# Kernel optimization log

Hardware: AMD Instinct MI355X
Metric: run time of the kernel (lower is better)

The kernel has to match this reference:

```python
import jax, jax.numpy as jnp
import numpy as np

MC = 16384
IND_T = 96
N_MAT = 4
N_STRIKES = 21


def _init_linear(key, fan_in, fan_out, prefix=()):
    k1, k2 = jax.random.split(key)
    lim = 1.0 / np.sqrt(fan_in)
    W = jax.random.uniform(k1, prefix + (fan_in, fan_out), minval=-lim, maxval=lim, dtype=jnp.float32)
    b = jax.random.uniform(k2, prefix + (fan_out,), minval=-lim, maxval=lim, dtype=jnp.float32)
    return W, b


def setup_inputs() -> dict:
    key = jax.random.key(0)
    ks = jax.random.split(key, 14)
    z = jax.random.normal(ks[0], (MC, IND_T), dtype=jnp.float32)
    zz = jax.random.normal(ks[1], (MC, IND_T), dtype=jnp.float32)
    timegrid = jnp.arange(IND_T + 1, dtype=jnp.float32) / 365.0  # daily grid
    maturities = jnp.array([24, 48, 72, 96], dtype=jnp.int32)    # in days
    strikes = jnp.linspace(0.8, 1.2, N_STRIKES, dtype=jnp.float32)
    sv_W1, sv_b1 = _init_linear(ks[2], 3, 100)
    sv_W2, sv_b2 = _init_linear(ks[3], 100, 100)
    sv_W3, sv_b3 = _init_linear(ks[4], 100, 1)
    vh_W1, vh_b1 = _init_linear(ks[5], 2, 20, (N_MAT,))
    vh_W2, vh_b2 = _init_linear(ks[6], 20, N_STRIKES, (N_MAT,))
    vd_W1, vd_b1 = _init_linear(ks[7], 1, 20)
    vd_W2, vd_b2 = _init_linear(ks[8], 20, 1)
    vv_W1, vv_b1 = _init_linear(ks[9], 1, 20)
    vv_W2, vv_b2 = _init_linear(ks[10], 20, 1)
    v0 = jax.random.uniform(ks[11], (1,), dtype=jnp.float32) * 0.1
    rho = jnp.ones((1,), dtype=jnp.float32) * -2.0
    return dict(S0=jnp.float32(1.0), rate=jnp.float32(0.05), z=z, zz=zz,
                timegrid=timegrid, strikes=strikes, v0=v0, rho=rho,
                sv_W1=sv_W1, sv_b1=sv_b1, sv_W2=sv_W2, sv_b2=sv_b2, sv_W3=sv_W3, sv_b3=sv_b3,
                vh_W1=vh_W1, vh_b1=vh_b1, vh_W2=vh_W2, vh_b2=vh_b2,
                vd_W1=vd_W1, vd_b1=vd_b1, vd_W2=vd_W2, vd_b2=vd_b2,
                vv_W1=vv_W1, vv_b1=vv_b1, vv_W2=vv_W2, vv_b2=vv_b2,
                maturities=maturities)


def reference(S0, rate, z, zz, timegrid, strikes, v0, rho,
              sv_W1, sv_b1, sv_W2, sv_b2, sv_W3, sv_b3,
              vh_W1, vh_b1, vh_W2, vh_b2,
              vd_W1, vd_b1, vd_W2, vd_b2,
              vv_W1, vv_b1, vv_W2, vv_b2,
              maturities):
    sg = jax.lax.stop_gradient
    mc = z.shape[0]
    n_mat = vh_W1.shape[0]
    n_strikes = strikes.shape[0]

    def s_vol(x):  # [MC,3] -> [MC,1], softplus output
        h1 = jax.nn.relu(x @ sv_W1 + sv_b1)
        h2 = jax.nn.relu(h1 @ sv_W2 + sv_b2)
        return jax.nn.softplus(h2 @ sv_W3 + sv_b3)

    def v_drift(v):  # [MC,1] -> [MC,1]
        return jax.nn.relu(v @ vd_W1 + vd_b1) @ vd_W2 + vd_b2

    def v_vol(v):  # [MC,1] -> [MC,1], softplus output
        return jax.nn.softplus(jax.nn.relu(v @ vv_W1 + vv_b1) @ vv_W2 + vv_b2)

    def vanilla_hedge_all(x):  # [MC,2] -> [MC, n_strikes, n_mat] (one net per maturity)
        h1 = jax.nn.relu(jnp.einsum('mi,kio->kmo', x, vh_W1) + vh_b1[:, None, :])
        out = jax.nn.softplus(jnp.einsum('kmo,koj->kmj', h1, vh_W2) + vh_b2[:, None, :])
        return jnp.transpose(out, (1, 2, 0))

    rho_t = jnp.tanh(rho)[0]
    days = jnp.round(timegrid * 365.0).astype(jnp.int32)       # [IND_T+1]
    le = days[1:, None] <= maturities[None, :]                  # [IND_T, n_mat]
    idx_net = jnp.argmax(le, axis=1)                            # first live maturity per step
    is_mat = jnp.any(days[1:, None] == maturities[None, :], axis=1)
    mat_idx = jnp.arange(n_mat)

    Slog0 = jnp.log(jnp.full((mc, 1), S0, dtype=jnp.float32))
    V0 = jnp.full((mc, 1), 1.0, dtype=jnp.float32) * jax.nn.sigmoid(v0)[0] * 0.5
    cv0 = jnp.zeros((mc, n_strikes, n_mat), dtype=jnp.float32)
    pv0 = jnp.zeros((n_mat, n_strikes), dtype=jnp.float32)

    xs = (z.T[:, :, None], zz.T[:, :, None], timegrid[:-1], timegrid[1:], idx_net, is_mat)

    def step(carry, x):
        Slog_old, V_old, cv, pv_h, pv_var = carry
        z_i, zz_i, t0, t1, idx, im = x
        h = t1 - t0
        sqh = jnp.sqrt(h)
        dW = sqh * z_i                                          # [MC,1]
        dB = rho_t * dW + jnp.sqrt(1.0 - rho_t ** 2) * sqh * zz_i
        ones_t = jnp.full((mc, 1), 1.0, dtype=jnp.float32) * t0
        pd = s_vol(jnp.concatenate([ones_t, Slog_old, V_old], axis=1))  # price diffusion
        cv_fwd = vanilla_hedge_all(jnp.concatenate([ones_t, sg(Slog_old)], axis=1))
        V_new = V_old + v_drift(V_old) * h + v_vol(V_old) * dB
        drift = rate - 0.5 * pd ** 2
        diff = pd * dW
        drift_c = 1.0 + jnp.abs(sg(drift)) * sqh                # tamed Euler
        diff_c = 1.0 + jnp.abs(sg(pd)) * sqh
        Slog_new = Slog_old + drift * h / drift_c + diff / diff_c
        S_new = jnp.exp(Slog_new)
        S_old = jnp.exp(Slog_old)
        dS = jnp.exp(-rate * t1) * S_new - jnp.exp(-rate * t0) * S_old  # [MC,1]
        mask = (mat_idx >= idx).astype(cv.dtype)                # live maturities only
        cv = cv + mask[None, None, :] * cv_fwd * sg(dS)[:, :, None]
        # hedged vanilla (call) prices collected at maturity steps
        payoff = jnp.exp(-rate * t1) * jnp.maximum(S_new - strikes[None, :], 0.0)
        price = payoff - cv[:, :, idx]                          # [MC, n_strikes]
        pv = jnp.mean(price, axis=0)
        pvar = jnp.var(price, axis=0, ddof=1)
        sel = (mat_idx == idx)[:, None] & im
        pv_h = jnp.where(sel, pv[None, :], pv_h)
        pv_var = jnp.where(sel, pvar[None, :], pv_var)
        return (Slog_new, V_new, cv, pv_h, pv_var), None

    (_, _, _, pv_h, pv_var), _ = jax.lax.scan(step, (Slog0, V0, cv0, pv0, pv0), xs)
    return jnp.stack([pv_h, pv_var])  # [2, n_mat, n_strikes]
```

## Files before the change

### kernel.cpp

```cpp
#include <hip/hip_runtime.h>
#include <hip/hip_bf16.h>
#include <math.h>


#define MC      16384
#define NSTEP   96
#define BLOCK   1024
#define NGROUP  256
#define NPAIR   84

typedef short bf16x8 __attribute__((ext_vector_type(8)));
typedef float f32x4  __attribute__((ext_vector_type(4)));

union U8 { uint4 u; bf16x8 v; };
union BF2U { __hip_bfloat162 b; unsigned u; };

__device__ __forceinline__ unsigned bf16rne(float x) {
    unsigned u = __float_as_uint(x);
    return (u + 0x7FFFu + ((u >> 16) & 1u)) >> 16;
}
__device__ __forceinline__ unsigned pk2(float lo, float hi) {
    BF2U t; t.b = __float22bfloat162_rn(make_float2(lo, hi));
    return t.u;
}
__device__ __forceinline__ float sp(float x) {
    return fmaxf(x, 0.f) + __logf(1.f + __expf(-fabsf(x)));
}

__global__ __launch_bounds__(BLOCK, 4)
void lsv_sim(const float* __restrict__ S0p,   const float* __restrict__ ratep,
             const float* __restrict__ z,     const float* __restrict__ zzg,
             const float* __restrict__ strikesg,
             const float* __restrict__ v0p,   const float* __restrict__ rhop,
             const float* __restrict__ svW1,  const float* __restrict__ svb1,
             const float* __restrict__ svW2,  const float* __restrict__ svb2,
             const float* __restrict__ svW3,  const float* __restrict__ svb3,
             const float* __restrict__ vhW1,  const float* __restrict__ vhb1,
             const float* __restrict__ vhW2,  const float* __restrict__ vhb2,
             const float* __restrict__ vdW1,  const float* __restrict__ vdb1,
             const float* __restrict__ vdW2,  const float* __restrict__ vdb2,
             const float* __restrict__ vvW1,  const float* __restrict__ vvb1,
             const float* __restrict__ vvW2,  const float* __restrict__ vvb2,
             const int*   __restrict__ mats,
             float* __restrict__ psum, float* __restrict__ psq)
{
    __shared__ __align__(16) unsigned short H1c[16 * 64 * 8];
    __shared__ __align__(16) float W1f[16 * 32];
    __shared__ __align__(16) float WH1f[16 * 32];
    __shared__ __align__(16) float B2T[128], W3T[128];
    __shared__ float RED[64 * 4];
    __shared__ float VDl[2][64], VVl[2][64];
    __shared__ float PSs[4][32], PSq[4][32];
    __shared__ float VW[128];

    const int tid  = threadIdx.x;
    const int lane = tid & 63;
    const int w    = __builtin_amdgcn_readfirstlane(tid >> 6);
    const int quad = lane >> 4;
    const int col  = lane & 15;
    const int gpath = blockIdx.x * 64 + lane;

    const int pt = w & 3;
    const int jg = w >> 2;
    const int hm = w >> 2;

    for (int e = tid; e < 128; e += BLOCK) {
        float v = 0.f;
        if      (e < 20)             v = vdW1[e];
        else if (e < 40)             v = vdb1[e - 20];
        else if (e < 60)             v = vdW2[e - 40];
        else if (e >= 64 && e < 84)  v = vvW1[e - 64];
        else if (e >= 84 && e < 104) v = vvb1[e - 84];
        else if (e >= 104 && e < 124)v = vvW2[e - 104];
        else if (e == 124)           v = vdb2[0];
        else if (e == 125)           v = vvb2[0];
        VW[e] = v;
        B2T[e] = (e < 100) ? svb2[e] : 0.f;
        W3T[e] = (e < 100) ? svW3[e] : 0.f;
    }
    for (int e = tid; e < 512; e += BLOCK) {
        const int kc2 = e >> 5, r5 = e & 31, grp = r5 >> 3, kk = kc2 * 8 + (r5 & 7);
        float v = 0.f;
        if (kk < 100) v = (grp == 0) ? svW1[kk] : (grp == 1) ? svW1[100 + kk]
                        : (grp == 2) ? svW1[200 + kk] : svb1[kk];
        W1f[e] = v;
    }
    for (int e = tid; e < 512; e += BLOCK) {
        const int hq = e >> 5, r5 = e & 31, grp = r5 >> 3;
        const int hmm = hq >> 2, qq = hq & 3;
        const int j = qq * 8 + (r5 & 7);
        float v = 0.f;
        if (j < 20 && grp < 3)
            v = (grp == 0) ? vhW1[hmm * 40 + j] : (grp == 1) ? vhW1[hmm * 40 + 20 + j]
                                                : vhb1[hmm * 20 + j];
        WH1f[e] = v;
    }

    const float rate  = ratep[0];
    const float S0    = S0p[0];
    const float rho_t = tanhf(rhop[0]);
    const float srho  = sqrtf(1.f - rho_t * rho_t);
    const float b3    = svb3[0];
    int matr[4];
#pragma unroll
    for (int k = 0; k < 4; k++) matr[k] = mats[k];

    bf16x8 Af[4][2];
#pragma unroll
    for (int c = 0; c < 4; c++)
#pragma unroll
        for (int t = 0; t < 2; t++) {
            U8 tt;
#pragma unroll
            for (int e2 = 0; e2 < 4; e2++) {
                const int k0 = 32 * c + 8 * quad + 2 * e2;
                const int j  = (2 * jg + t) * 16 + col;
                const float v0 = (k0     < 100 && j < 100) ? svW2[k0 * 100 + j]       : 0.f;
                const float v1 = (k0 + 1 < 100 && j < 100) ? svW2[(k0 + 1) * 100 + j] : 0.f;
                (&tt.u.x)[e2] = bf16rne(v0) | (bf16rne(v1) << 16);
            }
            Af[c][t] = tt.v;
        }
    bf16x8 Ah[2];
#pragma unroll
    for (int st = 0; st < 2; st++) {
        U8 tt;
#pragma unroll
        for (int e2 = 0; e2 < 4; e2++) {
            const int j0 = 8 * quad + 2 * e2, j1 = j0 + 1;
            const int s  = st * 16 + col;
            const float v0 = (j0 < 20 && s < 21) ? vhW2[hm * 420 + j0 * 21 + s] : 0.f;
            const float v1 = (j1 < 20 && s < 21) ? vhW2[hm * 420 + j1 * 21 + s] : 0.f;
            (&tt.u.x)[e2] = bf16rne(v0) | (bf16rne(v1) << 16);
        }
        Ah[st] = tt.v;
    }
    float b2h0[4], b2h1[4], K0a[4], K1a[4];
#pragma unroll
    for (int r = 0; r < 4; r++) {
        const int s0 = quad * 4 + r, s1 = 16 + quad * 4 + r;
        b2h0[r] = vhb2[hm * 21 + s0];
        K0a[r]  = strikesg[s0];
        b2h1[r] = (s1 < 21) ? vhb2[hm * 21 + s1] : 0.f;
        K1a[r]  = (s1 < 21) ? strikesg[s1] : 1e30f;
    }

    float Slog = __logf(S0);
    float S    = __expf(Slog);
    float V    = (1.f / (1.f + __expf(-v0p[0]))) * 0.5f;
    f32x4 cv0 = {0.f, 0.f, 0.f, 0.f};
    f32x4 cv1 = {0.f, 0.f, 0.f, 0.f};
    float Slog_prev = 0.f, dS_prev = 0.f, disc1_prev = 1.f, t0_prev = 0.f;
    int   idx_prev = 0;
    bool  im_prev  = false;

    const float* zrow  = z   + (size_t)gpath * NSTEP;
    const float* zzrow = zzg + (size_t)gpath * NSTEP;

    const int path = pt * 16 + col;
    const int kc   = jg * 4 + quad;

    __syncthreads();

    auto hedge_step = [&]() {
        if (hm >= idx_prev) {
            const float slp = __shfl(Slog_prev, path);
            U8 b;
#pragma unroll
            for (int hh = 0; hh < 2; hh++) {
                const float* Wp = WH1f + (hm * 4 + quad) * 32 + hh * 4;
                const float4 wt4 = *reinterpret_cast<const float4*>(Wp);
                const float4 ws4 = *reinterpret_cast<const float4*>(Wp + 8);
                const float4 bb4 = *reinterpret_cast<const float4*>(Wp + 16);
                const float x0 = fmaxf(bb4.x + t0_prev * wt4.x + slp * ws4.x, 0.f);
                const float x1 = fmaxf(bb4.y + t0_prev * wt4.y + slp * ws4.y, 0.f);
                const float x2 = fmaxf(bb4.z + t0_prev * wt4.z + slp * ws4.z, 0.f);
                const float x3 = fmaxf(bb4.w + t0_prev * wt4.w + slp * ws4.w, 0.f);
                (&b.u.x)[2 * hh]     = pk2(x0, x1);
                (&b.u.x)[2 * hh + 1] = pk2(x2, x3);
            }
            const f32x4 z4 = {0.f, 0.f, 0.f, 0.f};
            const f32x4 D0 = __builtin_amdgcn_mfma_f32_16x16x32_bf16(Ah[0], b.v, z4, 0, 0, 0);
            const f32x4 D1 = __builtin_amdgcn_mfma_f32_16x16x32_bf16(Ah[1], b.v, z4, 0, 0, 0);
            const float dsP = __shfl(dS_prev, path);
#pragma unroll
            for (int r = 0; r < 4; r++) {
                cv0[r] += sp(D0[r] + b2h0[r]) * dsP;
                cv1[r] += sp(D1[r] + b2h1[r]) * dsP;
            }
            if (im_prev && hm == idx_prev) {
                const float Sp = __shfl(S, path);
                float p0[4], q0[4], p1[4], q1[4];
#pragma unroll
                for (int r = 0; r < 4; r++) {
                    p0[r] = disc1_prev * fmaxf(Sp - K0a[r], 0.f) - cv0[r];
                    p1[r] = disc1_prev * fmaxf(Sp - K1a[r], 0.f) - cv1[r];
                    q0[r] = p0[r] * p0[r];
                    q1[r] = p1[r] * p1[r];
                }
#pragma unroll
                for (int o = 1; o <= 8; o <<= 1) {
#pragma unroll
                    for (int r = 0; r < 4; r++) {
                        p0[r] += __shfl_xor(p0[r], o);
                        q0[r] += __shfl_xor(q0[r], o);
                        p1[r] += __shfl_xor(p1[r], o);
                        q1[r] += __shfl_xor(q1[r], o);
                    }
                }
                if (col == 0) {
#pragma unroll
                    for (int r = 0; r < 4; r++) {
                        const int s0 = quad * 4 + r, s1 = 16 + quad * 4 + r;
                        PSs[pt][s0] = p0[r];  PSq[pt][s0] = q0[r];
                        if (s1 < 21) { PSs[pt][s1] = p1[r];  PSq[pt][s1] = q1[r]; }
                    }
                }
            }
        }
    };

    auto ps_reduce = [&]() {
        if (w == 0 && im_prev) {
            const int s = lane & 31;
            if (s < 21) {
                const float* src = (lane >= 32) ? &PSq[0][0] : &PSs[0][0];
                const float acc = src[s] + src[32 + s] + src[64 + s] + src[96 + s];
                float* dst = (lane >= 32) ? psq : psum;
                dst[(idx_prev * 21 + s) * NGROUP + blockIdx.x] = acc;
            }
        }
    };

    for (int i = 0; i < NSTEP; i++) {
        const float zi  = zrow[i];
        const float zzi = zzrow[i];

        const float t0    = (float)i       * (1.f / 365.f);
        const float t1    = (float)(i + 1) * (1.f / 365.f);
        const float h     = t1 - t0;
        const float sqh   = sqrtf(h);
        const float disc0 = __expf(-rate * t0);
        const float disc1 = __expf(-rate * t1);
        const int   day   = i + 1;
        const int   idx   = (day > matr[0]) + (day > matr[1]) + (day > matr[2]);
        const bool  im    = (day == matr[idx]);

        {
            const float slp = __shfl(Slog, path);
            const float vp  = __shfl(V, path);
            const float* Wp = W1f + kc * 32;
            uint4 o;
#pragma unroll
            for (int hh = 0; hh < 2; hh++) {
                const float4 a4 = *reinterpret_cast<const float4*>(Wp + hh * 4);
                const float4 b4 = *reinterpret_cast<const float4*>(Wp + 8 + hh * 4);
                const float4 c4 = *reinterpret_cast<const float4*>(Wp + 16 + hh * 4);
                const float4 d4 = *reinterpret_cast<const float4*>(Wp + 24 + hh * 4);
                const float x0 = fmaxf(d4.x + t0 * a4.x + slp * b4.x + vp * c4.x, 0.f);
                const float x1 = fmaxf(d4.y + t0 * a4.y + slp * b4.y + vp * c4.y, 0.f);
                const float x2 = fmaxf(d4.z + t0 * a4.z + slp * b4.z + vp * c4.z, 0.f);
                const float x3 = fmaxf(d4.w + t0 * a4.w + slp * b4.w + vp * c4.w, 0.f);
                (&o.x)[2 * hh]     = pk2(x0, x1);
                (&o.x)[2 * hh + 1] = pk2(x2, x3);
            }
            *reinterpret_cast<uint4*>(H1c + (kc * 64 + path) * 8) = o;
        }
        if (i > 0) hedge_step();
        if (w == 14) {
            float a2 = 0.f;
#pragma unroll
            for (int q5 = 0; q5 < 5; q5++) {
                const float4 w1 = *reinterpret_cast<const float4*>(VW + 4 * q5);
                const float4 b1 = *reinterpret_cast<const float4*>(VW + 20 + 4 * q5);
                const float4 w2 = *reinterpret_cast<const float4*>(VW + 40 + 4 * q5);
                a2 += fmaxf(V * w1.x + b1.x, 0.f) * w2.x;
                a2 += fmaxf(V * w1.y + b1.y, 0.f) * w2.y;
                a2 += fmaxf(V * w1.z + b1.z, 0.f) * w2.z;
                a2 += fmaxf(V * w1.w + b1.w, 0.f) * w2.w;
            }
            VDl[i & 1][lane] = a2;
        }
        if (w == 15) {
            float a2 = 0.f;
#pragma unroll
            for (int q5 = 0; q5 < 5; q5++) {
                const float4 w1 = *reinterpret_cast<const float4*>(VW + 64 + 4 * q5);
                const float4 b1 = *reinterpret_cast<const float4*>(VW + 84 + 4 * q5);
                const float4 w2 = *reinterpret_cast<const float4*>(VW + 104 + 4 * q5);
                a2 += fmaxf(V * w1.x + b1.x, 0.f) * w2.x;
                a2 += fmaxf(V * w1.y + b1.y, 0.f) * w2.y;
                a2 += fmaxf(V * w1.z + b1.z, 0.f) * w2.z;
                a2 += fmaxf(V * w1.w + b1.w, 0.f) * w2.w;
            }
            VVl[i & 1][lane] = a2;
        }
        __syncthreads();

        {
            f32x4 d0 = {0.f, 0.f, 0.f, 0.f};
            f32x4 d1 = {0.f, 0.f, 0.f, 0.f};
#pragma unroll
            for (int c = 0; c < 4; c++) {
                const bf16x8 b = *reinterpret_cast<const bf16x8*>(
                    H1c + ((quad + 4 * c) * 64 + path) * 8);
                d0 = __builtin_amdgcn_mfma_f32_16x16x32_bf16(Af[c][0], b, d0, 0, 0, 0);
                d1 = __builtin_amdgcn_mfma_f32_16x16x32_bf16(Af[c][1], b, d1, 0, 0, 0);
            }
            const int j0 = (2 * jg) * 16 + quad * 4;
            const float4 b2a = *reinterpret_cast<const float4*>(B2T + j0);
            const float4 w3a = *reinterpret_cast<const float4*>(W3T + j0);
            const float4 b2b = *reinterpret_cast<const float4*>(B2T + j0 + 16);
            const float4 w3b = *reinterpret_cast<const float4*>(W3T + j0 + 16);
            float acc = fmaxf(d0[0] + b2a.x, 0.f) * w3a.x
                      + fmaxf(d0[1] + b2a.y, 0.f) * w3a.y
                      + fmaxf(d0[2] + b2a.z, 0.f) * w3a.z
                      + fmaxf(d0[3] + b2a.w, 0.f) * w3a.w
                      + fmaxf(d1[0] + b2b.x, 0.f) * w3b.x
                      + fmaxf(d1[1] + b2b.y, 0.f) * w3b.y
                      + fmaxf(d1[2] + b2b.z, 0.f) * w3b.z
                      + fmaxf(d1[3] + b2b.w, 0.f) * w3b.w;
            acc += __shfl_xor(acc, 16);
            acc += __shfl_xor(acc, 32);
            if (quad == 0)
                RED[path * 4 + jg] = acc;
        }
        ps_reduce();
        __syncthreads();

        {
            const float4 rr = *reinterpret_cast<const float4*>(RED + lane * 4);
            const float pout = (rr.x + rr.y) + (rr.z + rr.w);
            const float pd = sp(pout + b3);
            const float vdv = VDl[i & 1][lane] + VW[124];
            const float vvv = sp(VVl[i & 1][lane] + VW[125]);
            const float dW = sqh * zi;
            const float dB = rho_t * dW + srho * sqh * zzi;
            const float Vn = V + vdv * h + vvv * dB;
            const float drift   = rate - 0.5f * pd * pd;
            const float diff    = pd * dW;
            const float drift_c = 1.f + fabsf(drift) * sqh;
            const float diff_c  = 1.f + fabsf(pd) * sqh;
            const float Sln = Slog + __fdividef(drift * h, drift_c) + __fdividef(diff, diff_c);
            const float Sn  = __expf(Sln);
            const float dS  = disc1 * Sn - disc0 * S;
            Slog_prev = Slog; dS_prev = dS; disc1_prev = disc1; t0_prev = t0;
            idx_prev = idx; im_prev = im;
            Slog = Sln; S = Sn; V = Vn;
        }
    }

    hedge_step();
    __syncthreads();
    ps_reduce();
}

__global__ void lsv_finalize(const float* __restrict__ psum,
                             const float* __restrict__ psq,
                             float* __restrict__ out)
{
    const int t = blockIdx.x * blockDim.x + threadIdx.x;
    if (t >= NPAIR) return;
    float s = 0.f, q = 0.f;
    for (int b = 0; b < NGROUP; b++) {
        s += psum[t * NGROUP + b];
        q += psq [t * NGROUP + b];
    }
    const float mean = s * (1.0f / (float)MC);
    const float var  = (q - (float)MC * mean * mean) * (1.0f / (float)(MC - 1));
    out[t]         = mean;
    out[NPAIR + t] = var;
}

extern "C" void kernel_launch(void* const* d_in, const int* in_sizes, int n_in,
                              void* d_out, int out_size, void* d_ws, size_t ws_size,
                              hipStream_t stream)
{
    const float* S0    = (const float*)d_in[0];
    const float* rate  = (const float*)d_in[1];
    const float* z     = (const float*)d_in[2];
    const float* zz    = (const float*)d_in[3];
    const float* strikes = (const float*)d_in[5];
    const float* v0    = (const float*)d_in[6];
    const float* rho   = (const float*)d_in[7];
    const float* svW1  = (const float*)d_in[8];
    const float* svb1  = (const float*)d_in[9];
    const float* svW2  = (const float*)d_in[10];
    const float* svb2  = (const float*)d_in[11];
    const float* svW3  = (const float*)d_in[12];
    const float* svb3  = (const float*)d_in[13];
    const float* vhW1  = (const float*)d_in[14];
    const float* vhb1  = (const float*)d_in[15];
    const float* vhW2  = (const float*)d_in[16];
    const float* vhb2  = (const float*)d_in[17];
    const float* vdW1  = (const float*)d_in[18];
    const float* vdb1  = (const float*)d_in[19];
    const float* vdW2  = (const float*)d_in[20];
    const float* vdb2  = (const float*)d_in[21];
    const float* vvW1  = (const float*)d_in[22];
    const float* vvb1  = (const float*)d_in[23];
    const float* vvW2  = (const float*)d_in[24];
    const float* vvb2  = (const float*)d_in[25];
    const int*   mats  = (const int*)d_in[26];

    float* psum = (float*)d_ws;
    float* psq  = psum + NPAIR * NGROUP;

    hipLaunchKernelGGL(lsv_sim, dim3(NGROUP), dim3(BLOCK), 0, stream,
                       S0, rate, z, zz, strikes, v0, rho,
                       svW1, svb1, svW2, svb2, svW3, svb3,
                       vhW1, vhb1, vhW2, vhb2,
                       vdW1, vdb1, vdW2, vdb2,
                       vvW1, vvb1, vvW2, vvb2,
                       mats, psum, psq);

    hipLaunchKernelGGL(lsv_finalize, dim3(1), dim3(128), 0, stream,
                       psum, psq, (float*)d_out);
}
```

Measured before the change: 436.6 us.

## Halve paths per block, precompute step tables, parallelize finalize reduction

Each block now simulates 32 paths with 512 threads, giving 512 blocks instead of 256 with 64 paths each. Per-warp roles and shared-memory strides are remapped to match. Per-step constants (t0, h, sqrt h, discounts, maturity index and flag) are precomputed into shared tables, hedge-net biases are folded into the MFMA accumulator, and the layer-2 bias/weight loads are hoisted out of the loop. The finalize kernel switches from a single serial thread per pair to one wavefront per pair with a shuffle reduction. Half of each wave's lanes duplicate path work, and the workspace doubles.

```diff
diff --git a/kernel.cpp b/kernel.cpp
--- a/kernel.cpp
+++ b/kernel.cpp
@@ -5,8 +5,8 @@
 
 #define MC      16384
 #define NSTEP   96
-#define BLOCK   1024
-#define NGROUP  256
+#define BLOCK   512
+#define NGROUP  512
 #define NPAIR   84
 
 typedef short bf16x8 __attribute__((ext_vector_type(8)));
@@ -44,25 +44,29 @@
              const int*   __restrict__ mats,
              float* __restrict__ psum, float* __restrict__ psq)
 {
-    __shared__ __align__(16) unsigned short H1c[16 * 64 * 8];
+    __shared__ __align__(16) unsigned short H1c[16 * 32 * 8];
     __shared__ __align__(16) float W1f[16 * 32];
     __shared__ __align__(16) float WH1f[16 * 32];
     __shared__ __align__(16) float B2T[128], W3T[128];
-    __shared__ float RED[64 * 4];
-    __shared__ float VDl[2][64], VVl[2][64];
-    __shared__ float PSs[4][32], PSq[4][32];
-    __shared__ float VW[128];
+    __shared__ __align__(16) float RED[32 * 4];
+    __shared__ __align__(16) float VDl[2][32], VVl[2][32];
+    __shared__ __align__(16) float PSs[2][32], PSq[2][32];
+    __shared__ __align__(16) float VW[128];
+    __shared__ __align__(16) float4 STEP[NSTEP];
+    __shared__ float D1T[NSTEP];
+    __shared__ int   ITAB[NSTEP];
 
     const int tid  = threadIdx.x;
     const int lane = tid & 63;
     const int w    = __builtin_amdgcn_readfirstlane(tid >> 6);
     const int quad = lane >> 4;
     const int col  = lane & 15;
-    const int gpath = blockIdx.x * 64 + lane;
-
-    const int pt = w & 3;
-    const int jg = w >> 2;
-    const int hm = w >> 2;
+    const int lp   = lane & 31;
+    const int gpath = blockIdx.x * 32 + lp;
+
+    const int pt = w & 1;
+    const int jg = w >> 1;
+    const int hm = w >> 1;
 
     for (int e = tid; e < 128; e += BLOCK) {
         float v = 0.f;
@@ -101,9 +105,20 @@
     const float rho_t = tanhf(rhop[0]);
     const float srho  = sqrtf(1.f - rho_t * rho_t);
     const float b3    = svb3[0];
-    int matr[4];
-#pragma unroll
-    for (int k = 0; k < 4; k++) matr[k] = mats[k];
+
+    if (tid < NSTEP) {
+        const int i = tid;
+        const float t0 = (float)i       * (1.f / 365.f);
+        const float t1 = (float)(i + 1) * (1.f / 365.f);
+        const float h  = t1 - t0;
+        STEP[i] = make_float4(t0, h, sqrtf(h), __expf(-rate * t0));
+        D1T[i]  = __expf(-rate * t1);
+        const int day = i + 1;
+        const int m0 = mats[0], m1 = mats[1], m2 = mats[2], m3 = mats[3];
+        const int idx = (day > m0) + (day > m1) + (day > m2);
+        const int mi  = (idx == 0) ? m0 : (idx == 1) ? m1 : (idx == 2) ? m2 : m3;
+        ITAB[i] = idx | ((day == mi) ? 256 : 0);
+    }
 
     bf16x8 Af[4][2];
 #pragma unroll
@@ -135,14 +150,15 @@
         }
         Ah[st] = tt.v;
     }
-    float b2h0[4], b2h1[4], K0a[4], K1a[4];
+    f32x4 c0h, c1h;
+    float K0a[4], K1a[4];
 #pragma unroll
     for (int r = 0; r < 4; r++) {
         const int s0 = quad * 4 + r, s1 = 16 + quad * 4 + r;
-        b2h0[r] = vhb2[hm * 21 + s0];
-        K0a[r]  = strikesg[s0];
-        b2h1[r] = (s1 < 21) ? vhb2[hm * 21 + s1] : 0.f;
-        K1a[r]  = (s1 < 21) ? strikesg[s1] : 1e30f;
+        c0h[r] = vhb2[hm * 21 + s0];
+        K0a[r] = strikesg[s0];
+        c1h[r] = (s1 < 21) ? vhb2[hm * 21 + s1] : 0.f;
+        K1a[r] = (s1 < 21) ? strikesg[s1] : 1e30f;
     }
 
     float Slog = __logf(S0);
@@ -150,9 +166,7 @@
     float V    = (1.f / (1.f + __expf(-v0p[0]))) * 0.5f;
     f32x4 cv0 = {0.f, 0.f, 0.f, 0.f};
     f32x4 cv1 = {0.f, 0.f, 0.f, 0.f};
-    float Slog_prev = 0.f, dS_prev = 0.f, disc1_prev = 1.f, t0_prev = 0.f;
-    int   idx_prev = 0;
-    bool  im_prev  = false;
+    float Slog_prev = 0.f, dS_prev = 0.f;
 
     const float* zrow  = z   + (size_t)gpath * NSTEP;
     const float* zzrow = zzg + (size_t)gpath * NSTEP;
@@ -162,8 +176,17 @@
 
     __syncthreads();
 
-    auto hedge_step = [&]() {
-        if (hm >= idx_prev) {
+    const int j0e = (2 * jg) * 16 + quad * 4;
+    const float4 b2a = *reinterpret_cast<const float4*>(B2T + j0e);
+    const float4 w3a = *reinterpret_cast<const float4*>(W3T + j0e);
+    const float4 b2b = *reinterpret_cast<const float4*>(B2T + j0e + 16);
+    const float4 w3b = *reinterpret_cast<const float4*>(W3T + j0e + 16);
+
+    auto hedge_step = [&](int ip) {
+        const int iv   = ITAB[ip];
+        const int idxp = iv & 0xff;
+        if (hm >= idxp) {
+            const float t0p = STEP[ip].x;
             const float slp = __shfl(Slog_prev, path);
             U8 b;
 #pragma unroll
@@ -172,29 +195,29 @@
                 const float4 wt4 = *reinterpret_cast<const float4*>(Wp);
                 const float4 ws4 = *reinterpret_cast<const float4*>(Wp + 8);
                 const float4 bb4 = *reinterpret_cast<const float4*>(Wp + 16);
-                const float x0 = fmaxf(bb4.x + t0_prev * wt4.x + slp * ws4.x, 0.f);
-                const float x1 = fmaxf(bb4.y + t0_prev * wt4.y + slp * ws4.y, 0.f);
-                const float x2 = fmaxf(bb4.z + t0_prev * wt4.z + slp * ws4.z, 0.f);
-                const float x3 = fmaxf(bb4.w + t0_prev * wt4.w + slp * ws4.w, 0.f);
+                const float x0 = fmaxf(bb4.x + t0p * wt4.x + slp * ws4.x, 0.f);
+                const float x1 = fmaxf(bb4.y + t0p * wt4.y + slp * ws4.y, 0.f);
+                const float x2 = fmaxf(bb4.z + t0p * wt4.z + slp * ws4.z, 0.f);
+                const float x3 = fmaxf(bb4.w + t0p * wt4.w + slp * ws4.w, 0.f);
                 (&b.u.x)[2 * hh]     = pk2(x0, x1);
                 (&b.u.x)[2 * hh + 1] = pk2(x2, x3);
             }
-            const f32x4 z4 = {0.f, 0.f, 0.f, 0.f};
-            const f32x4 D0 = __builtin_amdgcn_mfma_f32_16x16x32_bf16(Ah[0], b.v, z4, 0, 0, 0);
-            const f32x4 D1 = __builtin_amdgcn_mfma_f32_16x16x32_bf16(Ah[1], b.v, z4, 0, 0, 0);
+            const f32x4 D0 = __builtin_amdgcn_mfma_f32_16x16x32_bf16(Ah[0], b.v, c0h, 0, 0, 0);
+            const f32x4 D1 = __builtin_amdgcn_mfma_f32_16x16x32_bf16(Ah[1], b.v, c1h, 0, 0, 0);
             const float dsP = __shfl(dS_prev, path);
 #pragma unroll
             for (int r = 0; r < 4; r++) {
-                cv0[r] += sp(D0[r] + b2h0[r]) * dsP;
-                cv1[r] += sp(D1[r] + b2h1[r]) * dsP;
-            }
-            if (im_prev && hm == idx_prev) {
-                const float Sp = __shfl(S, path);
+                cv0[r] += sp(D0[r]) * dsP;
+                cv1[r] += sp(D1[r]) * dsP;
+            }
+            if ((iv & 256) && hm == idxp) {
+                const float Sp   = __shfl(S, path);
+                const float d1p  = D1T[ip];
                 float p0[4], q0[4], p1[4], q1[4];
 #pragma unroll
                 for (int r = 0; r < 4; r++) {
-                    p0[r] = disc1_prev * fmaxf(Sp - K0a[r], 0.f) - cv0[r];
-                    p1[r] = disc1_prev * fmaxf(Sp - K1a[r], 0.f) - cv1[r];
+                    p0[r] = d1p * fmaxf(Sp - K0a[r], 0.f) - cv0[r];
+                    p1[r] = d1p * fmaxf(Sp - K1a[r], 0.f) - cv1[r];
                     q0[r] = p0[r] * p0[r];
                     q1[r] = p1[r] * p1[r];
                 }
@@ -220,14 +243,17 @@
         }
     };
 
-    auto ps_reduce = [&]() {
-        if (w == 0 && im_prev) {
-            const int s = lane & 31;
-            if (s < 21) {
-                const float* src = (lane >= 32) ? &PSq[0][0] : &PSs[0][0];
-                const float acc = src[s] + src[32 + s] + src[64 + s] + src[96 + s];
-                float* dst = (lane >= 32) ? psq : psum;
-                dst[(idx_prev * 21 + s) * NGROUP + blockIdx.x] = acc;
+    auto ps_reduce = [&](int ip) {
+        if (w == 0) {
+            const int iv = ITAB[ip];
+            if (iv & 256) {
+                const int s = lane & 31;
+                if (s < 21) {
+                    const float* src = (lane >= 32) ? &PSq[0][0] : &PSs[0][0];
+                    const float acc = src[s] + src[32 + s];
+                    float* dst = (lane >= 32) ? psq : psum;
+                    dst[((iv & 0xff) * 21 + s) * NGROUP + blockIdx.x] = acc;
+                }
             }
         }
     };
@@ -235,20 +261,12 @@
     for (int i = 0; i < NSTEP; i++) {
         const float zi  = zrow[i];
         const float zzi = zzrow[i];
-
-        const float t0    = (float)i       * (1.f / 365.f);
-        const float t1    = (float)(i + 1) * (1.f / 365.f);
-        const float h     = t1 - t0;
-        const float sqh   = sqrtf(h);
-        const float disc0 = __expf(-rate * t0);
-        const float disc1 = __expf(-rate * t1);
-        const int   day   = i + 1;
-        const int   idx   = (day > matr[0]) + (day > matr[1]) + (day > matr[2]);
-        const bool  im    = (day == matr[idx]);
+        const float4 u  = STEP[i];
 
         {
             const float slp = __shfl(Slog, path);
             const float vp  = __shfl(V, path);
+            const float t0  = u.x;
             const float* Wp = W1f + kc * 32;
             uint4 o;
 #pragma unroll
@@ -264,10 +282,10 @@
                 (&o.x)[2 * hh]     = pk2(x0, x1);
                 (&o.x)[2 * hh + 1] = pk2(x2, x3);
             }
-            *reinterpret_cast<uint4*>(H1c + (kc * 64 + path) * 8) = o;
-        }
-        if (i > 0) hedge_step();
-        if (w == 14) {
+            *reinterpret_cast<uint4*>(H1c + (kc * 32 + path) * 8) = o;
+        }
+        if (i > 0) hedge_step(i - 1);
+        if (w == 0) {
             float a2 = 0.f;
 #pragma unroll
             for (int q5 = 0; q5 < 5; q5++) {
@@ -279,9 +297,9 @@
                 a2 += fmaxf(V * w1.z + b1.z, 0.f) * w2.z;
                 a2 += fmaxf(V * w1.w + b1.w, 0.f) * w2.w;
             }
-            VDl[i & 1][lane] = a2;
-        }
-        if (w == 15) {
+            if (lane < 32) VDl[i & 1][lane] = a2;
+        }
+        if (w == 1) {
             float a2 = 0.f;
 #pragma unroll
             for (int q5 = 0; q5 < 5; q5++) {
@@ -293,7 +311,7 @@
                 a2 += fmaxf(V * w1.z + b1.z, 0.f) * w2.z;
                 a2 += fmaxf(V * w1.w + b1.w, 0.f) * w2.w;
             }
-            VVl[i & 1][lane] = a2;
+            if (lane < 32) VVl[i & 1][lane] = a2;
         }
         __syncthreads();
 
@@ -303,15 +321,10 @@
 #pragma unroll
             for (int c = 0; c < 4; c++) {
                 const bf16x8 b = *reinterpret_cast<const bf16x8*>(
-                    H1c + ((quad + 4 * c) * 64 + path) * 8);
+                    H1c + ((quad + 4 * c) * 32 + path) * 8);
                 d0 = __builtin_amdgcn_mfma_f32_16x16x32_bf16(Af[c][0], b, d0, 0, 0, 0);
                 d1 = __builtin_amdgcn_mfma_f32_16x16x32_bf16(Af[c][1], b, d1, 0, 0, 0);
             }
-            const int j0 = (2 * jg) * 16 + quad * 4;
-            const float4 b2a = *reinterpret_cast<const float4*>(B2T + j0);
-            const float4 w3a = *reinterpret_cast<const float4*>(W3T + j0);
-            const float4 b2b = *reinterpret_cast<const float4*>(B2T + j0 + 16);
-            const float4 w3b = *reinterpret_cast<const float4*>(W3T + j0 + 16);
             float acc = fmaxf(d0[0] + b2a.x, 0.f) * w3a.x
                       + fmaxf(d0[1] + b2a.y, 0.f) * w3a.y
                       + fmaxf(d0[2] + b2a.z, 0.f) * w3a.z
@@ -325,51 +338,58 @@
             if (quad == 0)
                 RED[path * 4 + jg] = acc;
         }
-        ps_reduce();
+        if (i > 0) ps_reduce(i - 1);
         __syncthreads();
 
         {
-            const float4 rr = *reinterpret_cast<const float4*>(RED + lane * 4);
+            const float4 rr = *reinterpret_cast<const float4*>(RED + lp * 4);
             const float pout = (rr.x + rr.y) + (rr.z + rr.w);
             const float pd = sp(pout + b3);
-            const float vdv = VDl[i & 1][lane] + VW[124];
-            const float vvv = sp(VVl[i & 1][lane] + VW[125]);
+            const float vdv = VDl[i & 1][lp] + VW[124];
+            const float vvv = sp(VVl[i & 1][lp] + VW[125]);
+            const float sqh = u.z;
             const float dW = sqh * zi;
             const float dB = rho_t * dW + srho * sqh * zzi;
-            const float Vn = V + vdv * h + vvv * dB;
+            const float Vn = V + vdv * u.y + vvv * dB;
             const float drift   = rate - 0.5f * pd * pd;
             const float diff    = pd * dW;
             const float drift_c = 1.f + fabsf(drift) * sqh;
             const float diff_c  = 1.f + fabsf(pd) * sqh;
-            const float Sln = Slog + __fdividef(drift * h, drift_c) + __fdividef(diff, diff_c);
+            const float Sln = Slog + __fdividef(drift * u.y, drift_c) + __fdividef(diff, diff_c);
             const float Sn  = __expf(Sln);
-            const float dS  = disc1 * Sn - disc0 * S;
-            Slog_prev = Slog; dS_prev = dS; disc1_prev = disc1; t0_prev = t0;
-            idx_prev = idx; im_prev = im;
+            const float dS  = D1T[i] * Sn - u.w * S;
+            Slog_prev = Slog; dS_prev = dS;
             Slog = Sln; S = Sn; V = Vn;
         }
     }
 
-    hedge_step();
+    hedge_step(NSTEP - 1);
     __syncthreads();
-    ps_reduce();
+    ps_reduce(NSTEP - 1);
 }
 
 __global__ void lsv_finalize(const float* __restrict__ psum,
                              const float* __restrict__ psq,
                              float* __restrict__ out)
 {
-    const int t = blockIdx.x * blockDim.x + threadIdx.x;
-    if (t >= NPAIR) return;
+    const int t    = blockIdx.x;
+    const int lane = threadIdx.x;
     float s = 0.f, q = 0.f;
-    for (int b = 0; b < NGROUP; b++) {
+    for (int b = lane; b < NGROUP; b += 64) {
         s += psum[t * NGROUP + b];
         q += psq [t * NGROUP + b];
     }
-    const float mean = s * (1.0f / (float)MC);
-    const float var  = (q - (float)MC * mean * mean) * (1.0f / (float)(MC - 1));
-    out[t]         = mean;
-    out[NPAIR + t] = var;
+#pragma unroll
+    for (int o = 1; o <= 32; o <<= 1) {
+        s += __shfl_xor(s, o);
+        q += __shfl_xor(q, o);
+    }
+    if (lane == 0) {
+        const float mean = s * (1.0f / (float)MC);
+        const float var  = (q - (float)MC * mean * mean) * (1.0f / (float)(MC - 1));
+        out[t]         = mean;
+        out[NPAIR + t] = var;
+    }
 }
 
 extern "C" void kernel_launch(void* const* d_in, const int* in_sizes, int n_in,
@@ -414,6 +434,6 @@
                        vvW1, vvb1, vvW2, vvb2,
                        mats, psum, psq);
 
-    hipLaunchKernelGGL(lsv_finalize, dim3(1), dim3(128), 0, stream,
+    hipLaunchKernelGGL(lsv_finalize, dim3(NPAIR), dim3(64), 0, stream,
                        psum, psq, (float*)d_out);
 }
```

After: 435.7 us. No clear change (-0.2%).
